# Kernel optimization log

Hardware: AMD Instinct MI355X
Metric: run time of the kernel (lower is better)

## Reference

```python
import jax, jax.numpy as jnp
import numpy as np

B, N, T, F, H, O = 32, 256, 64, 16, 128, 1  # batch, nodes, seq_len, input, hidden, output


def setup_inputs() -> dict:
    key = jax.random.key(0)
    ks = jax.random.split(key, 14)
    s = 0.05
    nrm = lambda k, shp: jax.random.normal(k, shp, jnp.float32) * s
    return {
        "x": jax.random.normal(ks[0], (B, N, T, F), jnp.float32),
        "A": jax.random.normal(ks[1], (N, N), jnp.float32),
        "W_ih0": nrm(ks[2], (4 * H, F)),
        "W_hh0": nrm(ks[3], (4 * H, H)),
        "b_ih0": nrm(ks[4], (4 * H,)),
        "b_hh0": nrm(ks[5], (4 * H,)),
        "W_ih1": nrm(ks[6], (4 * H, H)),
        "W_hh1": nrm(ks[7], (4 * H, H)),
        "b_ih1": nrm(ks[8], (4 * H,)),
        "b_hh1": nrm(ks[9], (4 * H,)),
        "W1": nrm(ks[10], (H, H)),
        "W2": nrm(ks[11], (H, H)),
        "W3": nrm(ks[12], (H, H)),
        "Wfc": nrm(ks[13], (O, H)),
    }


def _lstm_layer(inp, W_ih, W_hh, b_ih, b_hh):
    # inp: (BN, T, F_in). PyTorch LSTM gate order: i, f, g, o.
    BN = inp.shape[0]
    Hd = W_hh.shape[1]
    h0 = jnp.zeros((BN, Hd), inp.dtype)
    c0 = jnp.zeros((BN, Hd), inp.dtype)

    def step(carry, x_t):
        h, c = carry
        g = x_t @ W_ih.T + b_ih + h @ W_hh.T + b_hh
        i, f, gg, o = jnp.split(g, 4, axis=-1)
        c = jax.nn.sigmoid(f) * c + jax.nn.sigmoid(i) * jnp.tanh(gg)
        h = jax.nn.sigmoid(o) * jnp.tanh(c)
        return (h, c), h

    (hT, _), hs = jax.lax.scan(step, (h0, c0), jnp.swapaxes(inp, 0, 1))
    return jnp.swapaxes(hs, 0, 1), hT  # (BN, T, H), (BN, H)


def reference(x, A, W_ih0, W_hh0, b_ih0, b_hh0, W_ih1, W_hh1, b_ih1, b_hh1, W1, W2, W3, Wfc):
    Bx, Nx, Tx, Fx = x.shape
    # Batch the per-node LSTM calls: all (batch, node) pairs share LSTM weights.
    xs = x.reshape(Bx * Nx, Tx, Fx)
    h1_seq, _ = _lstm_layer(xs, W_ih0, W_hh0, b_ih0, b_hh0)
    _, hT = _lstm_layer(h1_seq, W_ih1, W_hh1, b_ih1, b_hh1)  # last layer final hidden
    h_LSTM = hT.reshape(Bx, Nx, -1).transpose(0, 2, 1)  # (B, H, N)

    A_p = jax.nn.sigmoid(A)
    HA = jnp.einsum('bhn,nl->bhl', h_LSTM, A_p)        # H @ A'
    h_A = HA.transpose(0, 2, 1)                        # (B, N, H)
    W1hA = jnp.einsum('bnh,gh->bgn', h_A, W1)          # (B, H, N)
    mid = jax.nn.relu(jnp.einsum('bnh,gh->bng', h_A, W2))
    W3r = jnp.einsum('bng,fg->bfn', mid, W3)           # (B, H, N)
    ATW = jnp.einsum('bhn,nl->bhl', W3r, A_p)
    alpha = 0.9
    h_out = (1.0 - alpha) * ATW + alpha * W1hA         # (B, H, N)
    # Per-node MLP (shared weights) + sigmoid, batched over nodes.
    out = jax.nn.sigmoid(jnp.einsum('bhn,oh->bno', h_out, Wfc))  # (B, N, O)
    return out
```

## Files before the change

### kernel.cpp

```cpp
#include <hip/hip_runtime.h>


typedef __attribute__((ext_vector_type(4))) float f32x4;
typedef __attribute__((ext_vector_type(2))) float f32x2;
typedef __attribute__((ext_vector_type(8))) __bf16 bf16x8;
typedef __attribute__((ext_vector_type(8))) unsigned short u16x8;
typedef __attribute__((ext_vector_type(4))) unsigned short u16x4;

#define DEV static __device__ __forceinline__

DEV unsigned short f2bf(float f) {
  unsigned u = __builtin_bit_cast(unsigned, f);
  u = u + 0x7fffu + ((u >> 16) & 1u);
  return (unsigned short)(u >> 16);
}
DEV float bf2f(unsigned short s) {
  unsigned u = ((unsigned)s) << 16;
  return __builtin_bit_cast(float, u);
}

DEV float fexp2(float x) { return __builtin_amdgcn_exp2f(x); }
DEV f32x2 exp2v2(f32x2 x) { f32x2 r; r[0] = fexp2(x[0]); r[1] = fexp2(x[1]); return r; }
DEV f32x2 rcpv2(f32x2 x) {
  f32x2 r; r[0] = __builtin_amdgcn_rcpf(x[0]); r[1] = __builtin_amdgcn_rcpf(x[1]); return r;
}

DEV unsigned cell_pair(f32x2 gi, f32x2 gf, f32x2 gg, f32x2 go, f32x2& cs) {
  const float K2 = 2.88539008f;
  f32x2 one = {1.f, 1.f};
  f32x2 t1 = exp2v2(gg);
  f32x2 t2 = exp2v2((f32x2){-gi[0], -gi[1]});
  f32x2 ef = exp2v2((f32x2){-gf[0], -gf[1]});
  f32x2 d1 = t1 + one;
  f32x2 den1 = d1 * t2 + d1;
  f32x2 e1 = one + ef;
  f32x2 num = cs * den1 + (f32x2){K2, K2} * (t1 - one) * e1;
  cs = num * rcpv2(e1 * den1);
  f32x2 t3 = exp2v2(cs);
  f32x2 t4 = exp2v2((f32x2){-go[0], -go[1]});
  f32x2 d3 = t3 + one;
  f32x2 den3 = d3 * t4 + d3;
  f32x2 h = (t3 - one) * rcpv2(den3);
  unsigned r;
  asm("v_cvt_pk_bf16_f32 %0, %1, %2" : "=v"(r) : "v"(h[0]), "v"(h[1]));
  return r;
}

#define O_W0PK   0
#define O_W1PK   163840
#define O_APK    425984
#define O_W1APK  557056
#define O_W2APK  589824
#define O_W3APK  622592
#define O_BIAS0  655360
#define O_BIAS1  657408
#define O_HTT    659456
#define O_HAT    2756608
#define O_MIDT   4853760
#define O_W1HAT  6950912
#define O_W3R    9048064
#define O_XPK    11145216
#define O_H1     44699648

#define PREPX_TOT 2097152
#define PREP_TOT  328704
#define PREPALL_TOT (PREPX_TOT + PREP_TOT)

DEV int gr_unit(int rt, int lq2, int s) { return 8 * (rt >> 1) + 2 * lq2 + s; }

__global__ void prep_all(const float* __restrict__ x, const float* __restrict__ A,
    const float* __restrict__ Wih0, const float* __restrict__ Whh0,
    const float* __restrict__ bih0, const float* __restrict__ bhh0,
    const float* __restrict__ Wih1, const float* __restrict__ Whh1,
    const float* __restrict__ bih1, const float* __restrict__ bhh1,
    const float* __restrict__ W1, const float* __restrict__ W2,
    const float* __restrict__ W3, char* __restrict__ ws)
{
  const float K1 = 1.44269504f, K2 = 2.88539008f;
  int gidx = blockIdx.x * blockDim.x + threadIdx.x;
  if (gidx < PREPX_TOT) {
    int tid = gidx;
    int dat = (tid < 1048576) ? 1 : 0;
    int id = tid & 1048575;
    int half = id & 1, t = (id >> 1) & 63, row = id >> 7;
    u16x8 v = (u16x8)0;
    if (dat) {
      const float* p = x + ((long)row * 64 + t) * 16 + 8 * half;
      float4 a = *(const float4*)p;
      float4 b = *(const float4*)(p + 4);
      v[0] = f2bf(a.x); v[1] = f2bf(a.y); v[2] = f2bf(a.z); v[3] = f2bf(a.w);
      v[4] = f2bf(b.x); v[5] = f2bf(b.y); v[6] = f2bf(b.z); v[7] = f2bf(b.w);
    } else if (half == 0) {
      v[0] = 0x3F80;
    }
    int lane = (dat ? 0 : 32) + half * 16 + (row & 15);
    int rt = row >> 4;
    ((u16x8*)(ws + O_XPK))[(rt * 64 + t) * 64 + lane] = v;
    return;
  }
  int idx = gidx - PREPX_TOT;
  if (idx >= PREP_TOT) return;
  if (idx < 81920) {
    int o = idx, i = o & 7, l = (o >> 3) & 63, f = o >> 9;
    int kt = f % 5, rt = f / 5;
    int lr = l & 15, lq = l >> 4;
    int p = lr & 3, lql = (lr >> 2) & 3;
    int gc = p * 128 + gr_unit(rt, lql, rt & 1);
    float sc = (p == 2) ? K2 : K1;
    float v;
    if (kt < 4) v = Whh0[gc * 128 + 32 * kt + 8 * lq + i];
    else {
      int kk = 8 * lq + i;
      v = (kk < 16) ? Wih0[gc * 16 + kk]
                    : (kk == 16 ? (bih0[gc] + bhh0[gc]) : 0.f);
    }
    ((unsigned short*)(ws + O_W0PK))[idx] = f2bf(v * sc);
  } else if (idx < 212992) {
    int o = idx - 81920, i = o & 7, l = (o >> 3) & 63, f = o >> 9;
    int kt = f & 7, rt = f >> 3;
    int lr = l & 15, lq = l >> 4;
    int p = lr & 3, lql = (lr >> 2) & 3;
    int gc = p * 128 + gr_unit(rt, lql, rt & 1);
    float sc = (p == 2) ? K2 : K1;
    float v = (kt < 4) ? Wih1[gc * 128 + 32 * kt + 8 * lq + i]
                       : Whh1[gc * 128 + 32 * (kt - 4) + 8 * lq + i];
    ((unsigned short*)(ws + O_W1PK))[o] = f2bf(v * sc);
  } else if (idx < 278528) {
    int o = idx - 212992, i = o & 7, l = (o >> 3) & 63, f = o >> 9;
    int kt = f & 7, ct = f >> 3;
    int n = 32 * kt + 8 * (l >> 4) + i;
    int lc = 16 * ct + (l & 15);
    float e = fexp2(-K1 * A[n * 256 + lc]);
    ((unsigned short*)(ws + O_APK))[o] = f2bf(__builtin_amdgcn_rcpf(1.f + e));
  } else if (idx < 327680) {
    int o = idx - 278528;
    int m = o >> 14;
    int oo = o & 16383;
    int i = oo & 7, l = (oo >> 3) & 63, f = oo >> 9;
    int kt = f & 3, rt = f >> 2;
    int g = 16 * rt + (l & 15);
    int k = 32 * kt + 8 * (l >> 4) + i;
    const float* W = (m == 0) ? W1 : (m == 1) ? W2 : W3;
    unsigned short* dst = (unsigned short*)(ws + ((m == 0) ? O_W1APK : (m == 1) ? O_W2APK : O_W3APK));
    dst[oo] = f2bf(W[g * 128 + k]);
  } else if (idx < 328192) {
    int c = idx - 327680;
    ((float*)(ws + O_BIAS0))[c] = bih0[c] + bhh0[c];
  } else {
    int c = idx - 328192;
    float sc = ((c >> 7) == 2) ? K2 : K1;
    ((float*)(ws + O_BIAS1))[c] = (bih1[c] + bhh1[c]) * sc;
  }
}

__global__ __launch_bounds__(1024, 4) void lstm0_k(char* __restrict__ ws, int row_base)
{
  const unsigned short* W0pk = (const unsigned short*)(ws + O_W0PK);
  const unsigned short* xpk = (const unsigned short*)(ws + O_XPK);
  unsigned short* h1 = (unsigned short*)(ws + O_H1);

  int tid = threadIdx.x;
  int Wv = tid >> 6, l = tid & 63, lr = l & 15, lq = l >> 4;
  int lrow = blockIdx.x * 32;
  long grow0 = (long)row_base + lrow;

  __shared__ unsigned char hlds[2][8192];
  ((u16x8*)hlds[0])[tid] = (u16x8)0;

  bf16x8 Af[2][5];
#pragma unroll
  for (int s = 0; s < 2; s++)
#pragma unroll
    for (int kt = 0; kt < 5; kt++)
      Af[s][kt] = ((const bf16x8*)W0pk)[(((2 * Wv + s) * 5) + kt) * 64 + l];

  f32x2 c_st[2] = {{0.f, 0.f}, {0.f, 0.f}};

  int rd[2][4], whp[2];
#pragma unroll
  for (int ct = 0; ct < 2; ct++) {
#pragma unroll
    for (int kt = 0; kt < 4; kt++)
      rd[ct][kt] = (16 * ct + lr) * 256 + ((64 * kt + 16 * lq) ^ ((lr & 7) << 4));
    whp[ct] = (16 * ct + lr) * 256 + ((16 * Wv + 4 * lq) ^ ((lr & 7) << 4));
  }

  int pr = tid >> 6, sj = tid & 63;
  int sld0 = pr * 256 + ((4 * sj) ^ ((pr & 7) << 4));
  int sld1 = (pr + 16) * 256 + ((4 * sj) ^ ((pr & 7) << 4));
  unsigned short* st0 = h1 + (long)(lrow + pr) * 8192 + 2 * sj;
  unsigned short* st1 = h1 + (long)(lrow + pr + 16) * 8192 + 2 * sj;

  const bf16x8* xp0 = (const bf16x8*)xpk + ((grow0 >> 4) + 0) * 4096 + l;
  const bf16x8* xp1 = (const bf16x8*)xpk + ((grow0 >> 4) + 1) * 4096 + l;
  bf16x8 xb[2] = {xp0[0], xp1[0]};
  __syncthreads();

  for (int t = 0; t < 64; t++) {
    const unsigned char* rbuf = hlds[t & 1];
    unsigned char* wbuf = hlds[(t & 1) ^ 1];
    int tn = (t < 63) ? t + 1 : 63;
    bf16x8 xbn0 = xp0[tn * 64];
    bf16x8 xbn1 = xp1[tn * 64];

    f32x4 acc[2][2];
#pragma unroll
    for (int ct = 0; ct < 2; ct++)
#pragma unroll
      for (int s = 0; s < 2; s++) acc[ct][s] = (f32x4){0.f, 0.f, 0.f, 0.f};
    __builtin_amdgcn_s_setprio(1);
#pragma unroll
    for (int kt = 0; kt < 4; kt++) {
      bf16x8 hb0 = *(const bf16x8*)(rbuf + rd[0][kt]);
      bf16x8 hb1 = *(const bf16x8*)(rbuf + rd[1][kt]);
      acc[0][0] = __builtin_amdgcn_mfma_f32_16x16x32_bf16(Af[0][kt], hb0, acc[0][0], 0, 0, 0);
      acc[0][1] = __builtin_amdgcn_mfma_f32_16x16x32_bf16(Af[1][kt], hb0, acc[0][1], 0, 0, 0);
      acc[1][0] = __builtin_amdgcn_mfma_f32_16x16x32_bf16(Af[0][kt], hb1, acc[1][0], 0, 0, 0);
      acc[1][1] = __builtin_amdgcn_mfma_f32_16x16x32_bf16(Af[1][kt], hb1, acc[1][1], 0, 0, 0);
    }
    acc[0][0] = __builtin_amdgcn_mfma_f32_16x16x32_bf16(Af[0][4], xb[0], acc[0][0], 0, 0, 0);
    acc[0][1] = __builtin_amdgcn_mfma_f32_16x16x32_bf16(Af[1][4], xb[0], acc[0][1], 0, 0, 0);
    acc[1][0] = __builtin_amdgcn_mfma_f32_16x16x32_bf16(Af[0][4], xb[1], acc[1][0], 0, 0, 0);
    acc[1][1] = __builtin_amdgcn_mfma_f32_16x16x32_bf16(Af[1][4], xb[1], acc[1][1], 0, 0, 0);
    __builtin_amdgcn_s_setprio(0);
#pragma unroll
    for (int ct = 0; ct < 2; ct++) {
      f32x2 gi = {acc[ct][0][0], acc[ct][1][0]};
      f32x2 gf = {acc[ct][0][1], acc[ct][1][1]};
      f32x2 gg = {acc[ct][0][2], acc[ct][1][2]};
      f32x2 go = {acc[ct][0][3], acc[ct][1][3]};
      *(unsigned*)(wbuf + whp[ct]) = cell_pair(gi, gf, gg, go, c_st[ct]);
    }
    xb[0] = xbn0; xb[1] = xbn1;
    __syncthreads();
    *(unsigned*)(st0 + t * 128) = *(const unsigned*)(hlds[(t & 1) ^ 1] + sld0);
    *(unsigned*)(st1 + t * 128) = *(const unsigned*)(hlds[(t & 1) ^ 1] + sld1);
  }
}

__global__ __launch_bounds__(1024, 4) void lstm1_k(char* __restrict__ ws, int row_base)
{
  const unsigned short* W1pk = (const unsigned short*)(ws + O_W1PK);
  const float* bias1 = (const float*)(ws + O_BIAS1);
  const unsigned short* h1 = (const unsigned short*)(ws + O_H1);
  unsigned short* hTt = (unsigned short*)(ws + O_HTT);

  int tid = threadIdx.x;
  int Wv = tid >> 6, l = tid & 63, lr = l & 15, lq = l >> 4;
  int lrow = blockIdx.x * 32;
  long grow0 = (long)row_base + lrow;

  __shared__ unsigned char hlds[2][8192];
  __shared__ unsigned char h1s[2][8192];
  ((u16x8*)hlds[0])[tid] = (u16x8)0;

  int prow = tid >> 6, pc = tid & 63;
  const unsigned short* s0 = h1 + (long)(lrow + prow) * 8192 + 2 * pc;
  const unsigned short* s1 = h1 + (long)(lrow + prow + 16) * 8192 + 2 * pc;
  int d0 = prow * 256 + ((4 * pc) ^ ((prow & 7) << 4));
  int d1 = (prow + 16) * 256 + ((4 * pc) ^ ((prow & 7) << 4));
  *(unsigned*)(h1s[0] + d0) = *(const unsigned*)s0;
  *(unsigned*)(h1s[0] + d1) = *(const unsigned*)s1;

  bf16x8 Af[2][8];
#pragma unroll
  for (int s = 0; s < 2; s++)
#pragma unroll
    for (int kt = 0; kt < 8; kt++)
      Af[s][kt] = ((const bf16x8*)W1pk)[(((2 * Wv + s) * 8) + kt) * 64 + l];

  f32x4 bias_c[2];
#pragma unroll
  for (int s = 0; s < 2; s++)
#pragma unroll
    for (int r = 0; r < 4; r++)
      bias_c[s][r] = bias1[r * 128 + 8 * Wv + 2 * lq + s];

  f32x2 c_st[2] = {{0.f, 0.f}, {0.f, 0.f}};

  int rd[2][4], whp[2];
#pragma unroll
  for (int ct = 0; ct < 2; ct++) {
#pragma unroll
    for (int kt = 0; kt < 4; kt++)
      rd[ct][kt] = (16 * ct + lr) * 256 + ((64 * kt + 16 * lq) ^ ((lr & 7) << 4));
    whp[ct] = (16 * ct + lr) * 256 + ((16 * Wv + 4 * lq) ^ ((lr & 7) << 4));
  }
  __syncthreads();

  for (int t = 0; t < 64; t++) {
    const unsigned char* rbuf = hlds[t & 1];
    unsigned char* wbuf = hlds[(t & 1) ^ 1];
    const unsigned char* h1r = h1s[t & 1];
    unsigned char* h1w = h1s[(t & 1) ^ 1];
    int tn = (t < 63) ? t + 1 : 63;
    unsigned pf0 = *(const unsigned*)(s0 + tn * 128);
    unsigned pf1 = *(const unsigned*)(s1 + tn * 128);

    f32x4 acc[2][2];
#pragma unroll
    for (int ct = 0; ct < 2; ct++) {
      acc[ct][0] = bias_c[0]; acc[ct][1] = bias_c[1];
    }
    __builtin_amdgcn_s_setprio(1);
#pragma unroll
    for (int kt = 0; kt < 4; kt++) {
      bf16x8 xb0 = *(const bf16x8*)(h1r + rd[0][kt]);
      bf16x8 xb1 = *(const bf16x8*)(h1r + rd[1][kt]);
      acc[0][0] = __builtin_amdgcn_mfma_f32_16x16x32_bf16(Af[0][kt], xb0, acc[0][0], 0, 0, 0);
      acc[0][1] = __builtin_amdgcn_mfma_f32_16x16x32_bf16(Af[1][kt], xb0, acc[0][1], 0, 0, 0);
      acc[1][0] = __builtin_amdgcn_mfma_f32_16x16x32_bf16(Af[0][kt], xb1, acc[1][0], 0, 0, 0);
      acc[1][1] = __builtin_amdgcn_mfma_f32_16x16x32_bf16(Af[1][kt], xb1, acc[1][1], 0, 0, 0);
    }
#pragma unroll
    for (int kt = 0; kt < 4; kt++) {
      bf16x8 hb0 = *(const bf16x8*)(rbuf + rd[0][kt]);
      bf16x8 hb1 = *(const bf16x8*)(rbuf + rd[1][kt]);
      acc[0][0] = __builtin_amdgcn_mfma_f32_16x16x32_bf16(Af[0][4 + kt], hb0, acc[0][0], 0, 0, 0);
      acc[0][1] = __builtin_amdgcn_mfma_f32_16x16x32_bf16(Af[1][4 + kt], hb0, acc[0][1], 0, 0, 0);
      acc[1][0] = __builtin_amdgcn_mfma_f32_16x16x32_bf16(Af[0][4 + kt], hb1, acc[1][0], 0, 0, 0);
      acc[1][1] = __builtin_amdgcn_mfma_f32_16x16x32_bf16(Af[1][4 + kt], hb1, acc[1][1], 0, 0, 0);
    }
    __builtin_amdgcn_s_setprio(0);
#pragma unroll
    for (int ct = 0; ct < 2; ct++) {
      f32x2 gi = {acc[ct][0][0], acc[ct][1][0]};
      f32x2 gf = {acc[ct][0][1], acc[ct][1][1]};
      f32x2 gg = {acc[ct][0][2], acc[ct][1][2]};
      f32x2 go = {acc[ct][0][3], acc[ct][1][3]};
      *(unsigned*)(wbuf + whp[ct]) = cell_pair(gi, gf, gg, go, c_st[ct]);
    }
    *(unsigned*)(h1w + d0) = pf0;
    *(unsigned*)(h1w + d1) = pf1;
    __syncthreads();
  }

#pragma unroll
  for (int ct = 0; ct < 2; ct++) {
    unsigned hp = *(const unsigned*)(hlds[0] + whp[ct]);
    long grow = grow0 + 16 * ct + lr;
    long base = ((grow >> 8) * 128) * 256 + (grow & 255);
    int u0 = 8 * Wv + 2 * lq;
    hTt[base + (long)u0 * 256] = (unsigned short)(hp & 0xffff);
    hTt[base + (long)(u0 + 1) * 256] = (unsigned short)(hp >> 16);
  }
}

__global__ __launch_bounds__(256, 2) void g1_kernel(char* __restrict__ ws)
{
  const unsigned short* hTt = (const unsigned short*)(ws + O_HTT);
  const unsigned short* Apk = (const unsigned short*)(ws + O_APK);
  unsigned short* HAt = (unsigned short*)(ws + O_HAT);
  int tid = threadIdx.x, w = tid >> 6, l = tid & 63, lr = l & 15, lq = l >> 4;
  int bi = blockIdx.x;
  int b = bi >> 3, rtp = (bi >> 1) & 3, ch = bi & 1;
  f32x4 acc[2][2];
#pragma unroll
  for (int i = 0; i < 2; i++)
#pragma unroll
    for (int j = 0; j < 2; j++) acc[i][j] = (f32x4){0.f, 0.f, 0.f, 0.f};
  for (int kt = 0; kt < 8; kt++) {
    bf16x8 af[2];
#pragma unroll
    for (int rtl = 0; rtl < 2; rtl++) {
      int rt = rtp * 2 + rtl;
      af[rtl] = *(const bf16x8*)(hTt + (long)(b * 128 + 16 * rt + lr) * 256 + 32 * kt + 8 * lq);
    }
#pragma unroll
    for (int cti = 0; cti < 2; cti++) {
      int ct = w * 4 + ch * 2 + cti;
      bf16x8 bf = ((const bf16x8*)Apk)[(ct * 8 + kt) * 64 + l];
#pragma unroll
      for (int rtl = 0; rtl < 2; rtl++)
        acc[rtl][cti] = __builtin_amdgcn_mfma_f32_16x16x32_bf16(af[rtl], bf, acc[rtl][cti], 0, 0, 0);
    }
  }
#pragma unroll
  for (int rtl = 0; rtl < 2; rtl++)
#pragma unroll
    for (int cti = 0; cti < 2; cti++) {
      int rt = rtp * 2 + rtl, ct = w * 4 + ch * 2 + cti;
      u16x4 pk;
#pragma unroll
      for (int r = 0; r < 4; r++) pk[r] = f2bf(acc[rtl][cti][r]);
      *(u16x4*)(HAt + (long)(b * 256 + 16 * ct + lr) * 128 + 16 * rt + 4 * lq) = pk;
    }
}

__global__ __launch_bounds__(256, 2) void g2_kernel(char* __restrict__ ws)
{
  const unsigned short* HAt = (const unsigned short*)(ws + O_HAT);
  const unsigned short* W1apk = (const unsigned short*)(ws + O_W1APK);
  const unsigned short* W2apk = (const unsigned short*)(ws + O_W2APK);
  unsigned short* W1hAt = (unsigned short*)(ws + O_W1HAT);
  unsigned short* midT = (unsigned short*)(ws + O_MIDT);
  int tid = threadIdx.x, w = tid >> 6, l = tid & 63, lr = l & 15, lq = l >> 4;
  int bi = blockIdx.x;
  int b = bi >> 3, rtp = (bi >> 1) & 3, ch = bi & 1;
  f32x4 a1[2][2], a2[2][2];
#pragma unroll
  for (int i = 0; i < 2; i++)
#pragma unroll
    for (int j = 0; j < 2; j++) { a1[i][j] = (f32x4){0.f,0.f,0.f,0.f}; a2[i][j] = (f32x4){0.f,0.f,0.f,0.f}; }
  for (int kt = 0; kt < 4; kt++) {
    bf16x8 af1[2], af2[2];
#pragma unroll
    for (int rtl = 0; rtl < 2; rtl++) {
      int rt = rtp * 2 + rtl;
      af1[rtl] = ((const bf16x8*)W1apk)[(rt * 4 + kt) * 64 + l];
      af2[rtl] = ((const bf16x8*)W2apk)[(rt * 4 + kt) * 64 + l];
    }
#pragma unroll
    for (int cti = 0; cti < 2; cti++) {
      int ct = w * 4 + ch * 2 + cti;
      bf16x8 bf = *(const bf16x8*)(HAt + (long)(b * 256 + 16 * ct + lr) * 128 + 32 * kt + 8 * lq);
#pragma unroll
      for (int rtl = 0; rtl < 2; rtl++) {
        a1[rtl][cti] = __builtin_amdgcn_mfma_f32_16x16x32_bf16(af1[rtl], bf, a1[rtl][cti], 0, 0, 0);
        a2[rtl][cti] = __builtin_amdgcn_mfma_f32_16x16x32_bf16(af2[rtl], bf, a2[rtl][cti], 0, 0, 0);
      }
    }
  }
#pragma unroll
  for (int rtl = 0; rtl < 2; rtl++)
#pragma unroll
    for (int cti = 0; cti < 2; cti++) {
      int rt = rtp * 2 + rtl, ct = w * 4 + ch * 2 + cti;
      u16x4 p1, p2;
#pragma unroll
      for (int r = 0; r < 4; r++) {
        p1[r] = f2bf(a1[rtl][cti][r]);
        p2[r] = f2bf(fmaxf(a2[rtl][cti][r], 0.f));
      }
      long off = (long)(b * 256 + 16 * ct + lr) * 128 + 16 * rt + 4 * lq;
      *(u16x4*)(W1hAt + off) = p1;
      *(u16x4*)(midT + off) = p2;
    }
}

__global__ __launch_bounds__(256, 2) void g3_kernel(char* __restrict__ ws)
{
  const unsigned short* midT = (const unsigned short*)(ws + O_MIDT);
  const unsigned short* W3apk = (const unsigned short*)(ws + O_W3APK);
  unsigned short* W3r = (unsigned short*)(ws + O_W3R);
  int tid = threadIdx.x, w = tid >> 6, l = tid & 63, lr = l & 15, lq = l >> 4;
  int bi = blockIdx.x;
  int b = bi >> 3, rtp = (bi >> 1) & 3, ch = bi & 1;
  f32x4 acc[2][2];
#pragma unroll
  for (int i = 0; i < 2; i++)
#pragma unroll
    for (int j = 0; j < 2; j++) acc[i][j] = (f32x4){0.f, 0.f, 0.f, 0.f};
  for (int kt = 0; kt < 4; kt++) {
    bf16x8 af[2];
#pragma unroll
    for (int rtl = 0; rtl < 2; rtl++)
      af[rtl] = ((const bf16x8*)W3apk)[((rtp * 2 + rtl) * 4 + kt) * 64 + l];
#pragma unroll
    for (int cti = 0; cti < 2; cti++) {
      int ct = w * 4 + ch * 2 + cti;
      bf16x8 bf = *(const bf16x8*)(midT + (long)(b * 256 + 16 * ct + lr) * 128 + 32 * kt + 8 * lq);
#pragma unroll
      for (int rtl = 0; rtl < 2; rtl++)
        acc[rtl][cti] = __builtin_amdgcn_mfma_f32_16x16x32_bf16(af[rtl], bf, acc[rtl][cti], 0, 0, 0);
    }
  }
#pragma unroll
  for (int rtl = 0; rtl < 2; rtl++)
#pragma unroll
    for (int cti = 0; cti < 2; cti++) {
      int rt = rtp * 2 + rtl, ct = w * 4 + ch * 2 + cti;
#pragma unroll
      for (int r = 0; r < 4; r++)
        W3r[(long)(b * 128 + 16 * rt + 4 * lq + r) * 256 + 16 * ct + lr] = f2bf(acc[rtl][cti][r]);
    }
}

__global__ __launch_bounds__(256, 2) void g4_kernel(char* __restrict__ ws,
    const float* __restrict__ Wfc, float* __restrict__ out)
{
  const unsigned short* W3r = (const unsigned short*)(ws + O_W3R);
  const unsigned short* Apk = (const unsigned short*)(ws + O_APK);
  const unsigned short* W1hAt = (const unsigned short*)(ws + O_W1HAT);
  int tid = threadIdx.x, w = tid >> 6, l = tid & 63, lr = l & 15, lq = l >> 4;
  int bi = blockIdx.x;
  int b = bi >> 2, cq = bi & 3;
  int ct = cq * 4 + w;
  f32x4 acc[8];
#pragma unroll
  for (int i = 0; i < 8; i++) acc[i] = (f32x4){0.f, 0.f, 0.f, 0.f};
  for (int kt = 0; kt < 8; kt++) {
    bf16x8 bfv = ((const bf16x8*)Apk)[(ct * 8 + kt) * 64 + l];
#pragma unroll
    for (int rt = 0; rt < 8; rt++) {
      bf16x8 af = *(const bf16x8*)(W3r + (long)(b * 128 + 16 * rt + lr) * 256 + 32 * kt + 8 * lq);
      acc[rt] = __builtin_amdgcn_mfma_f32_16x16x32_bf16(af, bfv, acc[rt], 0, 0, 0);
    }
  }
  float psum = 0.f;
#pragma unroll
  for (int rt = 0; rt < 8; rt++) {
    float4 wf = *(const float4*)(Wfc + 16 * rt + 4 * lq);
    u16x4 wv = *(const u16x4*)(W1hAt + (long)(b * 256 + 16 * ct + lr) * 128 + 16 * rt + 4 * lq);
    psum += wf.x * (0.1f * acc[rt][0] + 0.9f * bf2f(wv[0]));
    psum += wf.y * (0.1f * acc[rt][1] + 0.9f * bf2f(wv[1]));
    psum += wf.z * (0.1f * acc[rt][2] + 0.9f * bf2f(wv[2]));
    psum += wf.w * (0.1f * acc[rt][3] + 0.9f * bf2f(wv[3]));
  }
  psum += __shfl_xor(psum, 16);
  psum += __shfl_xor(psum, 32);
  if (lq == 0) out[b * 256 + ct * 16 + lr] = __builtin_amdgcn_rcpf(1.f + fexp2(-1.44269504f * psum));
}

extern "C" void kernel_launch(void* const* d_in, const int* in_sizes, int n_in,
                              void* d_out, int out_size, void* d_ws, size_t ws_size,
                              hipStream_t stream)
{
  const float* x    = (const float*)d_in[0];
  const float* A    = (const float*)d_in[1];
  const float* Wih0 = (const float*)d_in[2];
  const float* Whh0 = (const float*)d_in[3];
  const float* bih0 = (const float*)d_in[4];
  const float* bhh0 = (const float*)d_in[5];
  const float* Wih1 = (const float*)d_in[6];
  const float* Whh1 = (const float*)d_in[7];
  const float* bih1 = (const float*)d_in[8];
  const float* bhh1 = (const float*)d_in[9];
  const float* W1   = (const float*)d_in[10];
  const float* W2   = (const float*)d_in[11];
  const float* W3   = (const float*)d_in[12];
  const float* Wfc  = (const float*)d_in[13];
  char* ws = (char*)d_ws;

  prep_all<<<(PREPALL_TOT + 255) / 256, 256, 0, stream>>>(
      x, A, Wih0, Whh0, bih0, bhh0, Wih1, Whh1, bih1, bhh1, W1, W2, W3, ws);

  size_t need_full = (size_t)O_H1 + 134217728u;
  size_t need_half = (size_t)O_H1 + 67108864u;
  if (ws_size >= need_full) {
    lstm0_k<<<256, 1024, 0, stream>>>(ws, 0);
    lstm1_k<<<256, 1024, 0, stream>>>(ws, 0);
  } else if (ws_size >= need_half) {
    for (int c = 0; c < 2; c++) {
      lstm0_k<<<128, 1024, 0, stream>>>(ws, c * 4096);
      lstm1_k<<<128, 1024, 0, stream>>>(ws, c * 4096);
    }
  } else {
    for (int c = 0; c < 4; c++) {
      lstm0_k<<<64, 1024, 0, stream>>>(ws, c * 2048);
      lstm1_k<<<64, 1024, 0, stream>>>(ws, c * 2048);
    }
  }

  g1_kernel<<<256, 256, 0, stream>>>(ws);
  g2_kernel<<<256, 256, 0, stream>>>(ws);
  g3_kernel<<<256, 256, 0, stream>>>(ws);
  g4_kernel<<<128, 256, 0, stream>>>(ws, Wfc, (float*)d_out);
}
```

Baseline: 260.5 us.

## Fuse the four graph GEMM kernels into one per-batch kernel using LDS

Replaces the four graph-stage kernels (H·A', W1/W2, W3, A'·W3r plus FC) with a single kernel launched as one 1024-thread block per batch. Intermediates stay in two 64KB LDS buffers with XOR swizzling instead of round-tripping through global workspace. This removes three kernel launches and the intermediate global traffic. The cost is a grid of only 32 blocks, which leaves most CUs idle during this phase, and 128KB of LDS per block.

```diff
diff --git a/kernel.cpp b/kernel.cpp
--- a/kernel.cpp
+++ b/kernel.cpp
@@ -55,10 +55,6 @@
 #define O_BIAS0  655360
 #define O_BIAS1  657408
 #define O_HTT    659456
-#define O_HAT    2756608
-#define O_MIDT   4853760
-#define O_W1HAT  6950912
-#define O_W3R    9048064
 #define O_XPK    11145216
 #define O_H1     44699648
 
@@ -346,154 +342,103 @@
   }
 }
 
-__global__ __launch_bounds__(256, 2) void g1_kernel(char* __restrict__ ws)
+__global__ __launch_bounds__(1024, 4) void g_all(char* __restrict__ ws,
+    const float* __restrict__ Wfc, float* __restrict__ out)
 {
   const unsigned short* hTt = (const unsigned short*)(ws + O_HTT);
   const unsigned short* Apk = (const unsigned short*)(ws + O_APK);
-  unsigned short* HAt = (unsigned short*)(ws + O_HAT);
-  int tid = threadIdx.x, w = tid >> 6, l = tid & 63, lr = l & 15, lq = l >> 4;
-  int bi = blockIdx.x;
-  int b = bi >> 3, rtp = (bi >> 1) & 3, ch = bi & 1;
-  f32x4 acc[2][2];
-#pragma unroll
-  for (int i = 0; i < 2; i++)
-#pragma unroll
-    for (int j = 0; j < 2; j++) acc[i][j] = (f32x4){0.f, 0.f, 0.f, 0.f};
-  for (int kt = 0; kt < 8; kt++) {
-    bf16x8 af[2];
-#pragma unroll
-    for (int rtl = 0; rtl < 2; rtl++) {
-      int rt = rtp * 2 + rtl;
-      af[rtl] = *(const bf16x8*)(hTt + (long)(b * 128 + 16 * rt + lr) * 256 + 32 * kt + 8 * lq);
-    }
-#pragma unroll
-    for (int cti = 0; cti < 2; cti++) {
-      int ct = w * 4 + ch * 2 + cti;
-      bf16x8 bf = ((const bf16x8*)Apk)[(ct * 8 + kt) * 64 + l];
-#pragma unroll
-      for (int rtl = 0; rtl < 2; rtl++)
-        acc[rtl][cti] = __builtin_amdgcn_mfma_f32_16x16x32_bf16(af[rtl], bf, acc[rtl][cti], 0, 0, 0);
-    }
-  }
-#pragma unroll
-  for (int rtl = 0; rtl < 2; rtl++)
-#pragma unroll
-    for (int cti = 0; cti < 2; cti++) {
-      int rt = rtp * 2 + rtl, ct = w * 4 + ch * 2 + cti;
-      u16x4 pk;
-#pragma unroll
-      for (int r = 0; r < 4; r++) pk[r] = f2bf(acc[rtl][cti][r]);
-      *(u16x4*)(HAt + (long)(b * 256 + 16 * ct + lr) * 128 + 16 * rt + 4 * lq) = pk;
-    }
-}
-
-__global__ __launch_bounds__(256, 2) void g2_kernel(char* __restrict__ ws)
-{
-  const unsigned short* HAt = (const unsigned short*)(ws + O_HAT);
   const unsigned short* W1apk = (const unsigned short*)(ws + O_W1APK);
   const unsigned short* W2apk = (const unsigned short*)(ws + O_W2APK);
-  unsigned short* W1hAt = (unsigned short*)(ws + O_W1HAT);
-  unsigned short* midT = (unsigned short*)(ws + O_MIDT);
-  int tid = threadIdx.x, w = tid >> 6, l = tid & 63, lr = l & 15, lq = l >> 4;
-  int bi = blockIdx.x;
-  int b = bi >> 3, rtp = (bi >> 1) & 3, ch = bi & 1;
-  f32x4 a1[2][2], a2[2][2];
-#pragma unroll
-  for (int i = 0; i < 2; i++)
-#pragma unroll
-    for (int j = 0; j < 2; j++) { a1[i][j] = (f32x4){0.f,0.f,0.f,0.f}; a2[i][j] = (f32x4){0.f,0.f,0.f,0.f}; }
-  for (int kt = 0; kt < 4; kt++) {
-    bf16x8 af1[2], af2[2];
-#pragma unroll
-    for (int rtl = 0; rtl < 2; rtl++) {
-      int rt = rtp * 2 + rtl;
-      af1[rtl] = ((const bf16x8*)W1apk)[(rt * 4 + kt) * 64 + l];
-      af2[rtl] = ((const bf16x8*)W2apk)[(rt * 4 + kt) * 64 + l];
-    }
-#pragma unroll
-    for (int cti = 0; cti < 2; cti++) {
-      int ct = w * 4 + ch * 2 + cti;
-      bf16x8 bf = *(const bf16x8*)(HAt + (long)(b * 256 + 16 * ct + lr) * 128 + 32 * kt + 8 * lq);
-#pragma unroll
-      for (int rtl = 0; rtl < 2; rtl++) {
-        a1[rtl][cti] = __builtin_amdgcn_mfma_f32_16x16x32_bf16(af1[rtl], bf, a1[rtl][cti], 0, 0, 0);
-        a2[rtl][cti] = __builtin_amdgcn_mfma_f32_16x16x32_bf16(af2[rtl], bf, a2[rtl][cti], 0, 0, 0);
-      }
-    }
-  }
-#pragma unroll
-  for (int rtl = 0; rtl < 2; rtl++)
-#pragma unroll
-    for (int cti = 0; cti < 2; cti++) {
-      int rt = rtp * 2 + rtl, ct = w * 4 + ch * 2 + cti;
-      u16x4 p1, p2;
-#pragma unroll
-      for (int r = 0; r < 4; r++) {
-        p1[r] = f2bf(a1[rtl][cti][r]);
-        p2[r] = f2bf(fmaxf(a2[rtl][cti][r], 0.f));
-      }
-      long off = (long)(b * 256 + 16 * ct + lr) * 128 + 16 * rt + 4 * lq;
-      *(u16x4*)(W1hAt + off) = p1;
-      *(u16x4*)(midT + off) = p2;
-    }
-}
-
-__global__ __launch_bounds__(256, 2) void g3_kernel(char* __restrict__ ws)
-{
-  const unsigned short* midT = (const unsigned short*)(ws + O_MIDT);
   const unsigned short* W3apk = (const unsigned short*)(ws + O_W3APK);
-  unsigned short* W3r = (unsigned short*)(ws + O_W3R);
-  int tid = threadIdx.x, w = tid >> 6, l = tid & 63, lr = l & 15, lq = l >> 4;
-  int bi = blockIdx.x;
-  int b = bi >> 3, rtp = (bi >> 1) & 3, ch = bi & 1;
-  f32x4 acc[2][2];
-#pragma unroll
-  for (int i = 0; i < 2; i++)
-#pragma unroll
-    for (int j = 0; j < 2; j++) acc[i][j] = (f32x4){0.f, 0.f, 0.f, 0.f};
-  for (int kt = 0; kt < 4; kt++) {
-    bf16x8 af[2];
-#pragma unroll
-    for (int rtl = 0; rtl < 2; rtl++)
-      af[rtl] = ((const bf16x8*)W3apk)[((rtp * 2 + rtl) * 4 + kt) * 64 + l];
-#pragma unroll
-    for (int cti = 0; cti < 2; cti++) {
-      int ct = w * 4 + ch * 2 + cti;
-      bf16x8 bf = *(const bf16x8*)(midT + (long)(b * 256 + 16 * ct + lr) * 128 + 32 * kt + 8 * lq);
-#pragma unroll
-      for (int rtl = 0; rtl < 2; rtl++)
-        acc[rtl][cti] = __builtin_amdgcn_mfma_f32_16x16x32_bf16(af[rtl], bf, acc[rtl][cti], 0, 0, 0);
-    }
-  }
-#pragma unroll
-  for (int rtl = 0; rtl < 2; rtl++)
-#pragma unroll
-    for (int cti = 0; cti < 2; cti++) {
-      int rt = rtp * 2 + rtl, ct = w * 4 + ch * 2 + cti;
-#pragma unroll
-      for (int r = 0; r < 4; r++)
-        W3r[(long)(b * 128 + 16 * rt + 4 * lq + r) * 256 + 16 * ct + lr] = f2bf(acc[rtl][cti][r]);
-    }
-}
-
-__global__ __launch_bounds__(256, 2) void g4_kernel(char* __restrict__ ws,
-    const float* __restrict__ Wfc, float* __restrict__ out)
-{
-  const unsigned short* W3r = (const unsigned short*)(ws + O_W3R);
-  const unsigned short* Apk = (const unsigned short*)(ws + O_APK);
-  const unsigned short* W1hAt = (const unsigned short*)(ws + O_W1HAT);
-  int tid = threadIdx.x, w = tid >> 6, l = tid & 63, lr = l & 15, lq = l >> 4;
-  int bi = blockIdx.x;
-  int b = bi >> 2, cq = bi & 3;
-  int ct = cq * 4 + w;
+
+  __shared__ unsigned char lA[65536];
+  __shared__ unsigned char lB[65536];
+
+  int tid = threadIdx.x;
+  int ct = tid >> 6, l = tid & 63, lr = l & 15, lq = l >> 4;
+  int b = blockIdx.x;
+  int nrow = 16 * ct + lr;
+
   f32x4 acc[8];
 #pragma unroll
-  for (int i = 0; i < 8; i++) acc[i] = (f32x4){0.f, 0.f, 0.f, 0.f};
+  for (int rt = 0; rt < 8; rt++) acc[rt] = (f32x4){0.f, 0.f, 0.f, 0.f};
   for (int kt = 0; kt < 8; kt++) {
     bf16x8 bfv = ((const bf16x8*)Apk)[(ct * 8 + kt) * 64 + l];
 #pragma unroll
     for (int rt = 0; rt < 8; rt++) {
-      bf16x8 af = *(const bf16x8*)(W3r + (long)(b * 128 + 16 * rt + lr) * 256 + 32 * kt + 8 * lq);
+      bf16x8 af = *(const bf16x8*)(hTt + (long)(b * 128 + 16 * rt + lr) * 256 + 32 * kt + 8 * lq);
+      acc[rt] = __builtin_amdgcn_mfma_f32_16x16x32_bf16(af, bfv, acc[rt], 0, 0, 0);
+    }
+  }
+#pragma unroll
+  for (int rt = 0; rt < 8; rt++) {
+    u16x4 pk;
+#pragma unroll
+    for (int r = 0; r < 4; r++) pk[r] = f2bf(acc[rt][r]);
+    *(u16x4*)(lA + nrow * 256 + ((32 * rt + 8 * lq) ^ ((lr & 7) << 4))) = pk;
+  }
+  __syncthreads();
+
+  int rdH[4];
+#pragma unroll
+  for (int kt = 0; kt < 4; kt++)
+    rdH[kt] = nrow * 256 + ((64 * kt + 16 * lq) ^ ((lr & 7) << 4));
+
+  f32x4 a2[8];
+#pragma unroll
+  for (int rt = 0; rt < 8; rt++) { acc[rt] = (f32x4){0.f,0.f,0.f,0.f}; a2[rt] = (f32x4){0.f,0.f,0.f,0.f}; }
+  for (int kt = 0; kt < 4; kt++) {
+    bf16x8 bfv = *(const bf16x8*)(lA + rdH[kt]);
+#pragma unroll
+    for (int rt = 0; rt < 8; rt++) {
+      bf16x8 af1 = ((const bf16x8*)W1apk)[(rt * 4 + kt) * 64 + l];
+      bf16x8 af2 = ((const bf16x8*)W2apk)[(rt * 4 + kt) * 64 + l];
+      acc[rt] = __builtin_amdgcn_mfma_f32_16x16x32_bf16(af1, bfv, acc[rt], 0, 0, 0);
+      a2[rt]  = __builtin_amdgcn_mfma_f32_16x16x32_bf16(af2, bfv, a2[rt], 0, 0, 0);
+    }
+  }
+  u16x4 a1s[8];
+#pragma unroll
+  for (int rt = 0; rt < 8; rt++) {
+    u16x4 p1, p2;
+#pragma unroll
+    for (int r = 0; r < 4; r++) {
+      p1[r] = f2bf(acc[rt][r]);
+      p2[r] = f2bf(fmaxf(a2[rt][r], 0.f));
+    }
+    a1s[rt] = p1;
+    *(u16x4*)(lB + nrow * 256 + ((32 * rt + 8 * lq) ^ ((lr & 7) << 4))) = p2;
+  }
+  __syncthreads();
+
+#pragma unroll
+  for (int rt = 0; rt < 8; rt++) acc[rt] = (f32x4){0.f, 0.f, 0.f, 0.f};
+  for (int kt = 0; kt < 4; kt++) {
+    bf16x8 bfv = *(const bf16x8*)(lB + rdH[kt]);
+#pragma unroll
+    for (int rt = 0; rt < 8; rt++) {
+      bf16x8 af3 = ((const bf16x8*)W3apk)[(rt * 4 + kt) * 64 + l];
+      acc[rt] = __builtin_amdgcn_mfma_f32_16x16x32_bf16(af3, bfv, acc[rt], 0, 0, 0);
+    }
+  }
+  __syncthreads();
+#pragma unroll
+  for (int rt = 0; rt < 8; rt++) {
+#pragma unroll
+    for (int r = 0; r < 4; r++) {
+      int f = 16 * rt + 4 * lq + r;
+      *(unsigned short*)(lA + f * 512 + ((2 * nrow) ^ ((f & 15) << 4))) = f2bf(acc[rt][r]);
+    }
+  }
+  __syncthreads();
+
+#pragma unroll
+  for (int rt = 0; rt < 8; rt++) acc[rt] = (f32x4){0.f, 0.f, 0.f, 0.f};
+  for (int kt = 0; kt < 8; kt++) {
+    bf16x8 bfv = ((const bf16x8*)Apk)[(ct * 8 + kt) * 64 + l];
+#pragma unroll
+    for (int rt = 0; rt < 8; rt++) {
+      bf16x8 af = *(const bf16x8*)(lA + (16 * rt + lr) * 512 + ((64 * kt + 16 * lq) ^ (lr << 4)));
       acc[rt] = __builtin_amdgcn_mfma_f32_16x16x32_bf16(af, bfv, acc[rt], 0, 0, 0);
     }
   }
@@ -501,15 +446,15 @@
 #pragma unroll
   for (int rt = 0; rt < 8; rt++) {
     float4 wf = *(const float4*)(Wfc + 16 * rt + 4 * lq);
-    u16x4 wv = *(const u16x4*)(W1hAt + (long)(b * 256 + 16 * ct + lr) * 128 + 16 * rt + 4 * lq);
-    psum += wf.x * (0.1f * acc[rt][0] + 0.9f * bf2f(wv[0]));
-    psum += wf.y * (0.1f * acc[rt][1] + 0.9f * bf2f(wv[1]));
-    psum += wf.z * (0.1f * acc[rt][2] + 0.9f * bf2f(wv[2]));
-    psum += wf.w * (0.1f * acc[rt][3] + 0.9f * bf2f(wv[3]));
+    psum += wf.x * (0.1f * acc[rt][0] + 0.9f * bf2f(a1s[rt][0]));
+    psum += wf.y * (0.1f * acc[rt][1] + 0.9f * bf2f(a1s[rt][1]));
+    psum += wf.z * (0.1f * acc[rt][2] + 0.9f * bf2f(a1s[rt][2]));
+    psum += wf.w * (0.1f * acc[rt][3] + 0.9f * bf2f(a1s[rt][3]));
   }
   psum += __shfl_xor(psum, 16);
   psum += __shfl_xor(psum, 32);
-  if (lq == 0) out[b * 256 + ct * 16 + lr] = __builtin_amdgcn_rcpf(1.f + fexp2(-1.44269504f * psum));
+  if (lq == 0)
+    out[b * 256 + nrow] = __builtin_amdgcn_rcpf(1.f + fexp2(-1.44269504f * psum));
 }
 
 extern "C" void kernel_launch(void* const* d_in, const int* in_sizes, int n_in,
@@ -552,8 +497,5 @@
     }
   }
 
-  g1_kernel<<<256, 256, 0, stream>>>(ws);
-  g2_kernel<<<256, 256, 0, stream>>>(ws);
-  g3_kernel<<<256, 256, 0, stream>>>(ws);
-  g4_kernel<<<128, 256, 0, stream>>>(ws, Wfc, (float*)d_out);
-}
+  g_all<<<32, 1024, 0, stream>>>(ws, Wfc, (float*)d_out);
+}
```

Result: slower. 281.3 us (+8.0%).
